# Kernel optimization log

Measured on AMD Instinct MI355X. Metric: run time of the kernel, lower is better.

The kernel has to match this reference:

```python
import jax, jax.numpy as jnp
import numpy as np

N, D, C, P = 4096, 512, 100, 64
EPS_COS = 1e-8   # torch cosine_similarity norm clamp
EPS_INV = 1e-5   # module's 1/(d + 1e-5)


def setup_inputs() -> dict:
    key = jax.random.key(0)
    k1, k2, k3, k4 = jax.random.split(key, 4)
    feats = jax.random.normal(k1, (N, D), dtype=jnp.float32)
    protos = jax.random.normal(k2, (C, P, D), dtype=jnp.float32)
    cls_ids = jax.random.randint(k3, (N,), 0, C)
    proto_labels = jax.random.randint(k4, (C, P), 0, 1000)
    return {"feats": feats, "protos": protos, "cls_ids": cls_ids,
            "proto_labels": proto_labels}


def reference(feats, protos, cls_ids, proto_labels):
    # Gather each box's class-conditional prototype set: [N, P, D]
    p = protos[cls_ids]
    pl = proto_labels[cls_ids]                       # [N, P]

    # cosine distance: 1 - f.p / (max(|f|,eps) * max(|p|,eps))
    dot = jnp.einsum('nd,npd->np', feats, p)         # [N, P]
    fnorm = jnp.maximum(jnp.linalg.norm(feats, axis=-1, keepdims=True), EPS_COS)
    pnorm = jnp.maximum(jnp.linalg.norm(p, axis=-1), EPS_COS)
    d_cos = 1.0 - dot / (fnorm * pnorm)

    diff = feats[:, None, :] - p                     # [N, P, D]
    d_l1 = jnp.mean(jnp.abs(diff), axis=-1)          # F.l1_loss (mean)
    d_l2 = jnp.mean(diff * diff, axis=-1)            # F.mse_loss (mean)

    dists = jnp.stack([d_cos, d_l1, d_l2], axis=1)   # [N, 3, P]
    probs = jax.nn.softmax(1.0 / (dists + EPS_INV), axis=-1).mean(axis=1)  # [N, P]

    idx = jnp.argmax(probs, axis=-1)                 # [N]
    labels = jnp.take_along_axis(pl, idx[:, None], axis=1)[:, 0]
    return labels, probs
```

## Files before the change

### kernel.cpp

```cpp
#include <hip/hip_runtime.h>

#define D 512
#define P 64
#define WPB 4
#define NB 2
#define MAXC 256
#define EPS_COS 1e-8f
#define EPS_INV 1e-5f

__device__ __forceinline__ float wave_sum(float v) {
#pragma unroll
    for (int m = 32; m >= 1; m >>= 1) v += __shfl_xor(v, m, 64);
    return v;
}

__global__ __launch_bounds__(256) void proto_norm_kernel(
    const float* __restrict__ protos, float* __restrict__ pp, int rows)
{
    const int lane = threadIdx.x & 63;
    const int wave = threadIdx.x >> 6;
    const int r = blockIdx.x * WPB + wave;
    if (r >= rows) return;
    const float* row = protos + (size_t)r * D;
    const float4 a = *(const float4*)(row + lane * 4);
    const float4 b = *(const float4*)(row + 256 + lane * 4);
    float s = a.x*a.x + a.y*a.y + a.z*a.z + a.w*a.w
            + b.x*b.x + b.y*b.y + b.z*b.z + b.w*b.w;
    s = wave_sum(s);
    if (lane == 0) pp[r] = s;
}

__global__ __launch_bounds__(1024) void build_groups_kernel(
    const int* __restrict__ cls_ids, int* __restrict__ slots,
    int* __restrict__ gcount, int N, int C)
{
    __shared__ int cnt[MAXC], base[MAXC], fill[MAXC];
    __shared__ int sG;
    const int tid = threadIdx.x;
    for (int c = tid; c < C; c += 1024) { cnt[c] = 0; fill[c] = 0; }
    __syncthreads();
    for (int n = tid; n < N; n += 1024) atomicAdd(&cnt[cls_ids[n]], 1);
    __syncthreads();
    if (tid == 0) {
        int gb = 0;
        for (int c = 0; c < C; ++c) { base[c] = gb; gb += (cnt[c] + NB - 1) / NB; }
        sG = gb;
        gcount[0] = gb;
    }
    __syncthreads();
    const int G = sG;
    for (int i = tid; i < G * NB; i += 1024) slots[i] = -1;
    __syncthreads();
    for (int n = tid; n < N; n += 1024) {
        const int c = cls_ids[n];
        const int p = atomicAdd(&fill[c], 1);
        slots[base[c] * NB + p] = n;
    }
}

__device__ __forceinline__ void box_epilogue(
    float r_dot, float r_l1, float ff, float s_pp, int myp,
    float& prob_o, int& bidx_o)
{
    const float fnorm = fmaxf(sqrtf(ff),   EPS_COS);
    const float pnorm = fmaxf(sqrtf(s_pp), EPS_COS);
    const float d_cos = 1.0f - r_dot / (fnorm * pnorm);
    const float d_l1  = r_l1 * (1.0f / (float)D);
    const float d_l2  = (ff - 2.0f * r_dot + s_pp) * (1.0f / (float)D);

    float s[3];
    s[0] = 1.0f / (d_cos + EPS_INV);
    s[1] = 1.0f / (d_l1  + EPS_INV);
    s[2] = 1.0f / (d_l2  + EPS_INV);

    float prob = 0.f;
#pragma unroll
    for (int i = 0; i < 3; ++i) {
        float m = s[i];
#pragma unroll
        for (int w = 32; w >= 1; w >>= 1) m = fmaxf(m, __shfl_xor(m, w, 64));
        const float e = expf(s[i] - m);
        const float denom = wave_sum(e);
        prob += e / denom;
    }
    prob *= (1.0f / 3.0f);

    float best = prob;
    int   bidx = myp;
#pragma unroll
    for (int w = 32; w >= 1; w >>= 1) {
        const float ov = __shfl_xor(best, w, 64);
        const int   oi = __shfl_xor(bidx, w, 64);
        if (ov > best || (ov == best && oi < bidx)) { best = ov; bidx = oi; }
    }
    prob_o = prob;
    bidx_o = bidx;
}

__global__ __launch_bounds__(WPB * 64) void proto_probs_kernel(
    const float* __restrict__ feats,
    const float* __restrict__ protos,
    const int*   __restrict__ cls_ids,
    const int*   __restrict__ proto_labels,
    const float* __restrict__ ppbuf,
    const int*   __restrict__ slots,
    const int*   __restrict__ gcount,
    float* __restrict__ out,
    int N)
{
    const int lane = threadIdx.x & 63;
    const int wave = threadIdx.x >> 6;

    const int nb  = gridDim.x;
    const int q   = nb >> 3, r = nb & 7;
    const int xcd = blockIdx.x & 7, bix = blockIdx.x >> 3;
    const int swz = (xcd < r ? xcd * (q + 1) : r * (q + 1) + (xcd - r) * q) + bix;

    const int g = swz * WPB + wave;
    if (g >= gcount[0]) return;

    const int b0 = slots[g * NB + 0];
    const int b1 = slots[g * NB + 1];
    const bool v1 = (b1 >= 0);
    const int n0 = b0;
    const int n1 = v1 ? b1 : b0;

    const int cls = cls_ids[n0];
    const float* fa = feats  + (size_t)n0 * D;
    const float* fb = feats  + (size_t)n1 * D;
    const float* pr = protos + (size_t)cls * (P * D);

    const float4 a0 = *(const float4*)(fa + lane * 4);
    const float4 a1 = *(const float4*)(fa + 256 + lane * 4);
    const float4 c0 = *(const float4*)(fb + lane * 4);
    const float4 c1 = *(const float4*)(fb + 256 + lane * 4);

    float ffa = a0.x*a0.x + a0.y*a0.y + a0.z*a0.z + a0.w*a0.w
              + a1.x*a1.x + a1.y*a1.y + a1.z*a1.z + a1.w*a1.w;
    float ffb = c0.x*c0.x + c0.y*c0.y + c0.z*c0.z + c0.w*c0.w
              + c1.x*c1.x + c1.y*c1.y + c1.z*c1.z + c1.w*c1.w;
    ffa = wave_sum(ffa);
    ffb = wave_sum(ffb);

    const int jsel = (lane >> 3) & 7;
    const int gown = lane & 7;
    const bool hi32 = (lane & 32) != 0;
    const bool hi16 = (lane & 16) != 0;
    const bool hi8  = (lane & 8)  != 0;

    float rdA = 0.f, rlA = 0.f, rdB = 0.f, rlB = 0.f;

    for (int gg = 0; gg < 8; ++gg) {
        float pdA[8], plA[8], pdB[8], plB[8];
#pragma unroll
        for (int j = 0; j < 8; ++j) {
            const float* row = pr + (size_t)(8 * gg + j) * D;
            const float4 q0 = *(const float4*)(row + lane * 4);
            const float4 q1 = *(const float4*)(row + 256 + lane * 4);
            float dA, lA, dB, lB, t;
            dA  = a0.x*q0.x; t = a0.x - q0.x; lA  = fabsf(t);
            dA += a0.y*q0.y; t = a0.y - q0.y; lA += fabsf(t);
            dA += a0.z*q0.z; t = a0.z - q0.z; lA += fabsf(t);
            dA += a0.w*q0.w; t = a0.w - q0.w; lA += fabsf(t);
            dA += a1.x*q1.x; t = a1.x - q1.x; lA += fabsf(t);
            dA += a1.y*q1.y; t = a1.y - q1.y; lA += fabsf(t);
            dA += a1.z*q1.z; t = a1.z - q1.z; lA += fabsf(t);
            dA += a1.w*q1.w; t = a1.w - q1.w; lA += fabsf(t);
            dB  = c0.x*q0.x; t = c0.x - q0.x; lB  = fabsf(t);
            dB += c0.y*q0.y; t = c0.y - q0.y; lB += fabsf(t);
            dB += c0.z*q0.z; t = c0.z - q0.z; lB += fabsf(t);
            dB += c0.w*q0.w; t = c0.w - q0.w; lB += fabsf(t);
            dB += c1.x*q1.x; t = c1.x - q1.x; lB += fabsf(t);
            dB += c1.y*q1.y; t = c1.y - q1.y; lB += fabsf(t);
            dB += c1.z*q1.z; t = c1.z - q1.z; lB += fabsf(t);
            dB += c1.w*q1.w; t = c1.w - q1.w; lB += fabsf(t);
            pdA[j] = dA; plA[j] = lA; pdB[j] = dB; plB[j] = lB;
        }
#pragma unroll
        for (int k = 0; k < 4; ++k) {
            const float sdA = hi32 ? pdA[k] : pdA[k + 4];
            const float slA = hi32 ? plA[k] : plA[k + 4];
            const float sdB = hi32 ? pdB[k] : pdB[k + 4];
            const float slB = hi32 ? plB[k] : plB[k + 4];
            const float rd0 = __shfl_xor(sdA, 32, 64);
            const float rl0 = __shfl_xor(slA, 32, 64);
            const float rd1 = __shfl_xor(sdB, 32, 64);
            const float rl1 = __shfl_xor(slB, 32, 64);
            pdA[k] = (hi32 ? pdA[k + 4] : pdA[k]) + rd0;
            plA[k] = (hi32 ? plA[k + 4] : plA[k]) + rl0;
            pdB[k] = (hi32 ? pdB[k + 4] : pdB[k]) + rd1;
            plB[k] = (hi32 ? plB[k + 4] : plB[k]) + rl1;
        }
#pragma unroll
        for (int k = 0; k < 2; ++k) {
            const float sdA = hi16 ? pdA[k] : pdA[k + 2];
            const float slA = hi16 ? plA[k] : plA[k + 2];
            const float sdB = hi16 ? pdB[k] : pdB[k + 2];
            const float slB = hi16 ? plB[k] : plB[k + 2];
            const float rd0 = __shfl_xor(sdA, 16, 64);
            const float rl0 = __shfl_xor(slA, 16, 64);
            const float rd1 = __shfl_xor(sdB, 16, 64);
            const float rl1 = __shfl_xor(slB, 16, 64);
            pdA[k] = (hi16 ? pdA[k + 2] : pdA[k]) + rd0;
            plA[k] = (hi16 ? plA[k + 2] : plA[k]) + rl0;
            pdB[k] = (hi16 ? pdB[k + 2] : pdB[k]) + rd1;
            plB[k] = (hi16 ? plB[k + 2] : plB[k]) + rl1;
        }
        {
            const float sdA = hi8 ? pdA[0] : pdA[1];
            const float slA = hi8 ? plA[0] : plA[1];
            const float sdB = hi8 ? pdB[0] : pdB[1];
            const float slB = hi8 ? plB[0] : plB[1];
            const float rd0 = __shfl_xor(sdA, 8, 64);
            const float rl0 = __shfl_xor(slA, 8, 64);
            const float rd1 = __shfl_xor(sdB, 8, 64);
            const float rl1 = __shfl_xor(slB, 8, 64);
            pdA[0] = (hi8 ? pdA[1] : pdA[0]) + rd0;
            plA[0] = (hi8 ? plA[1] : plA[0]) + rl0;
            pdB[0] = (hi8 ? pdB[1] : pdB[0]) + rd1;
            plB[0] = (hi8 ? plB[1] : plB[0]) + rl1;
        }
#pragma unroll
        for (int m = 4; m >= 1; m >>= 1) {
            pdA[0] += __shfl_xor(pdA[0], m, 64);
            plA[0] += __shfl_xor(plA[0], m, 64);
            pdB[0] += __shfl_xor(pdB[0], m, 64);
            plB[0] += __shfl_xor(plB[0], m, 64);
        }
        if (gown == gg) { rdA = pdA[0]; rlA = plA[0]; rdB = pdB[0]; rlB = plB[0]; }
    }

    const int myp = 8 * gown + jsel;
    const float s_pp = ppbuf[cls * P + myp];

    float probA; int bidxA;
    box_epilogue(rdA, rlA, ffa, s_pp, myp, probA, bidxA);
    out[(size_t)N + (size_t)n0 * P + myp] = probA;
    if (lane == 0) out[n0] = (float)proto_labels[cls * P + bidxA];

    if (v1) {
        float probB; int bidxB;
        box_epilogue(rdB, rlB, ffb, s_pp, myp, probB, bidxB);
        out[(size_t)N + (size_t)n1 * P + myp] = probB;
        if (lane == 0) out[n1] = (float)proto_labels[cls * P + bidxB];
    }
}

extern "C" void kernel_launch(void* const* d_in, const int* in_sizes, int n_in,
                              void* d_out, int out_size, void* d_ws, size_t ws_size,
                              hipStream_t stream) {
    const float* feats        = (const float*)d_in[0];
    const float* protos       = (const float*)d_in[1];
    const int*   cls_ids      = (const int*)d_in[2];
    const int*   proto_labels = (const int*)d_in[3];
    float* out = (float*)d_out;

    const int N    = in_sizes[2];
    const int rows = in_sizes[1] / D;
    const int C    = rows / P;

    float* pp     = (float*)d_ws;
    int*   gcount = (int*)((char*)d_ws + (size_t)rows * sizeof(float));
    int*   slots  = gcount + 1;

    const int Gmax    = (N + C * (NB - 1)) / NB;
    const int mblocks = (Gmax + WPB - 1) / WPB;

    proto_norm_kernel<<<(rows + WPB - 1) / WPB, WPB * 64, 0, stream>>>(
        protos, pp, rows);
    build_groups_kernel<<<1, 1024, 0, stream>>>(cls_ids, slots, gcount, N, C);
    proto_probs_kernel<<<mblocks, WPB * 64, 0, stream>>>(
        feats, protos, cls_ids, proto_labels, pp, slots, gcount, out, N);
}
```

Measured before the change: 119.2 us.

## Split each box-pair's D dimension across two waves and merge prep kernels

The prototype-norm and grouping kernels are fused into one launch, with the grouping block using a parallel prefix scan instead of a serial loop. The main kernel now assigns two waves to each box pair, each handling half of D, and combines their partial dot, L1 and norm sums through shared memory after a block barrier. This doubles the number of waves working on the same total work, reducing per-wave latency and register pressure. It also removes one kernel launch, at the cost of a __syncthreads and shared-memory exchange.

Measured after the change: 130.8 us. +9.7%, slower.

```diff
diff --git a/kernel.cpp b/kernel.cpp
--- a/kernel.cpp
+++ b/kernel.cpp
@@ -4,6 +4,7 @@
 #define P 64
 #define WPB 4
 #define NB 2
+#define PPB 2
 #define MAXC 256
 #define EPS_COS 1e-8f
 #define EPS_INV 1e-5f
@@ -14,47 +15,54 @@
     return v;
 }
 
-__global__ __launch_bounds__(256) void proto_norm_kernel(
-    const float* __restrict__ protos, float* __restrict__ pp, int rows)
+__global__ __launch_bounds__(256) void prep_kernel(
+    const float* __restrict__ protos, float* __restrict__ pp, int rows,
+    const int* __restrict__ cls_ids, int* __restrict__ slots,
+    int* __restrict__ gcount, int N, int C, int normBlocks)
 {
-    const int lane = threadIdx.x & 63;
-    const int wave = threadIdx.x >> 6;
-    const int r = blockIdx.x * WPB + wave;
-    if (r >= rows) return;
-    const float* row = protos + (size_t)r * D;
-    const float4 a = *(const float4*)(row + lane * 4);
-    const float4 b = *(const float4*)(row + 256 + lane * 4);
-    float s = a.x*a.x + a.y*a.y + a.z*a.z + a.w*a.w
-            + b.x*b.x + b.y*b.y + b.z*b.z + b.w*b.w;
-    s = wave_sum(s);
-    if (lane == 0) pp[r] = s;
-}
-
-__global__ __launch_bounds__(1024) void build_groups_kernel(
-    const int* __restrict__ cls_ids, int* __restrict__ slots,
-    int* __restrict__ gcount, int N, int C)
-{
-    __shared__ int cnt[MAXC], base[MAXC], fill[MAXC];
-    __shared__ int sG;
+    if ((int)blockIdx.x < normBlocks) {
+        const int lane = threadIdx.x & 63;
+        const int wave = threadIdx.x >> 6;
+        const int r = blockIdx.x * WPB + wave;
+        if (r >= rows) return;
+        const float* row = protos + (size_t)r * D;
+        const float4 a = *(const float4*)(row + lane * 4);
+        const float4 b = *(const float4*)(row + 256 + lane * 4);
+        float s = a.x*a.x + a.y*a.y + a.z*a.z + a.w*a.w
+                + b.x*b.x + b.y*b.y + b.z*b.z + b.w*b.w;
+        s = wave_sum(s);
+        if (lane == 0) pp[r] = s;
+        return;
+    }
+
+    __shared__ int cnt[MAXC], bas[MAXC], fil[MAXC];
+    __shared__ int sv[256];
     const int tid = threadIdx.x;
-    for (int c = tid; c < C; c += 1024) { cnt[c] = 0; fill[c] = 0; }
-    __syncthreads();
-    for (int n = tid; n < N; n += 1024) atomicAdd(&cnt[cls_ids[n]], 1);
-    __syncthreads();
-    if (tid == 0) {
-        int gb = 0;
-        for (int c = 0; c < C; ++c) { base[c] = gb; gb += (cnt[c] + NB - 1) / NB; }
-        sG = gb;
-        gcount[0] = gb;
-    }
-    __syncthreads();
-    const int G = sG;
-    for (int i = tid; i < G * NB; i += 1024) slots[i] = -1;
-    __syncthreads();
-    for (int n = tid; n < N; n += 1024) {
+    for (int c = tid; c < MAXC; c += 256) { cnt[c] = 0; fil[c] = 0; }
+    __syncthreads();
+    for (int n = tid; n < N; n += 256) atomicAdd(&cnt[cls_ids[n]], 1);
+    __syncthreads();
+    int v = 0;
+    if (tid < C) v = (cnt[tid] + NB - 1) / NB;
+    sv[tid] = v;
+    __syncthreads();
+#pragma unroll
+    for (int off = 1; off < 256; off <<= 1) {
+        const int t = (tid >= off) ? sv[tid - off] : 0;
+        __syncthreads();
+        sv[tid] += t;
+        __syncthreads();
+    }
+    const int G = sv[255];
+    if (tid < C) bas[tid] = sv[tid] - v;
+    if (tid == 0) gcount[0] = G;
+    __syncthreads();
+    for (int i = tid; i < G * NB; i += 256) slots[i] = -1;
+    __syncthreads();
+    for (int n = tid; n < N; n += 256) {
         const int c = cls_ids[n];
-        const int p = atomicAdd(&fill[c], 1);
-        slots[base[c] * NB + p] = n;
+        const int p = atomicAdd(&fil[c], 1);
+        slots[bas[c] * NB + p] = n;
     }
 }
 
@@ -97,7 +105,7 @@
     bidx_o = bidx;
 }
 
-__global__ __launch_bounds__(WPB * 64) void proto_probs_kernel(
+__global__ __launch_bounds__(PPB * 2 * 64) void proto_probs_kernel(
     const float* __restrict__ feats,
     const float* __restrict__ protos,
     const int*   __restrict__ cls_ids,
@@ -108,39 +116,24 @@
     float* __restrict__ out,
     int N)
 {
-    const int lane = threadIdx.x & 63;
-    const int wave = threadIdx.x >> 6;
-
-    const int nb  = gridDim.x;
-    const int q   = nb >> 3, r = nb & 7;
+    const int lane   = threadIdx.x & 63;
+    const int wave   = threadIdx.x >> 6;
+    const int pairId = wave >> 1;
+    const int sub    = wave & 1;
+
+    const int nbk = gridDim.x;
+    const int q   = nbk >> 3, r = nbk & 7;
     const int xcd = blockIdx.x & 7, bix = blockIdx.x >> 3;
     const int swz = (xcd < r ? xcd * (q + 1) : r * (q + 1) + (xcd - r) * q) + bix;
 
-    const int g = swz * WPB + wave;
-    if (g >= gcount[0]) return;
-
-    const int b0 = slots[g * NB + 0];
-    const int b1 = slots[g * NB + 1];
-    const bool v1 = (b1 >= 0);
-    const int n0 = b0;
-    const int n1 = v1 ? b1 : b0;
-
-    const int cls = cls_ids[n0];
-    const float* fa = feats  + (size_t)n0 * D;
-    const float* fb = feats  + (size_t)n1 * D;
-    const float* pr = protos + (size_t)cls * (P * D);
-
-    const float4 a0 = *(const float4*)(fa + lane * 4);
-    const float4 a1 = *(const float4*)(fa + 256 + lane * 4);
-    const float4 c0 = *(const float4*)(fb + lane * 4);
-    const float4 c1 = *(const float4*)(fb + 256 + lane * 4);
-
-    float ffa = a0.x*a0.x + a0.y*a0.y + a0.z*a0.z + a0.w*a0.w
-              + a1.x*a1.x + a1.y*a1.y + a1.z*a1.z + a1.w*a1.w;
-    float ffb = c0.x*c0.x + c0.y*c0.y + c0.z*c0.z + c0.w*c0.w
-              + c1.x*c1.x + c1.y*c1.y + c1.z*c1.z + c1.w*c1.w;
-    ffa = wave_sum(ffa);
-    ffb = wave_sum(ffb);
+    const int g = swz * PPB + pairId;
+    const int G = gcount[0];
+    int b0 = -1, b1 = -1;
+    if (g < G) { b0 = slots[NB * g]; b1 = slots[NB * g + 1]; }
+    const bool act = (b0 >= 0);
+    const bool v1  = (b1 >= 0);
+    const int n0 = act ? b0 : 0;
+    const int n1 = v1 ? b1 : n0;
 
     const int jsel = (lane >> 3) & 7;
     const int gown = lane & 7;
@@ -148,101 +141,119 @@
     const bool hi16 = (lane & 16) != 0;
     const bool hi8  = (lane & 8)  != 0;
 
-    float rdA = 0.f, rlA = 0.f, rdB = 0.f, rlB = 0.f;
-
-    for (int gg = 0; gg < 8; ++gg) {
-        float pdA[8], plA[8], pdB[8], plB[8];
-#pragma unroll
-        for (int j = 0; j < 8; ++j) {
-            const float* row = pr + (size_t)(8 * gg + j) * D;
-            const float4 q0 = *(const float4*)(row + lane * 4);
-            const float4 q1 = *(const float4*)(row + 256 + lane * 4);
-            float dA, lA, dB, lB, t;
-            dA  = a0.x*q0.x; t = a0.x - q0.x; lA  = fabsf(t);
-            dA += a0.y*q0.y; t = a0.y - q0.y; lA += fabsf(t);
-            dA += a0.z*q0.z; t = a0.z - q0.z; lA += fabsf(t);
-            dA += a0.w*q0.w; t = a0.w - q0.w; lA += fabsf(t);
-            dA += a1.x*q1.x; t = a1.x - q1.x; lA += fabsf(t);
-            dA += a1.y*q1.y; t = a1.y - q1.y; lA += fabsf(t);
-            dA += a1.z*q1.z; t = a1.z - q1.z; lA += fabsf(t);
-            dA += a1.w*q1.w; t = a1.w - q1.w; lA += fabsf(t);
-            dB  = c0.x*q0.x; t = c0.x - q0.x; lB  = fabsf(t);
-            dB += c0.y*q0.y; t = c0.y - q0.y; lB += fabsf(t);
-            dB += c0.z*q0.z; t = c0.z - q0.z; lB += fabsf(t);
-            dB += c0.w*q0.w; t = c0.w - q0.w; lB += fabsf(t);
-            dB += c1.x*q1.x; t = c1.x - q1.x; lB += fabsf(t);
-            dB += c1.y*q1.y; t = c1.y - q1.y; lB += fabsf(t);
-            dB += c1.z*q1.z; t = c1.z - q1.z; lB += fabsf(t);
-            dB += c1.w*q1.w; t = c1.w - q1.w; lB += fabsf(t);
-            pdA[j] = dA; plA[j] = lA; pdB[j] = dB; plB[j] = lB;
+    float rdA = 0.f, rlA = 0.f, rdB = 0.f, rlB = 0.f, ffa = 0.f, ffb = 0.f;
+    int cls = 0;
+
+    __shared__ float4 xch[PPB][2][64];
+    __shared__ float  xff[PPB][2][2];
+
+    if (act) {
+        cls = cls_ids[n0];
+        const float* fa = feats  + (size_t)n0 * D + sub * (D / 2);
+        const float* fb = feats  + (size_t)n1 * D + sub * (D / 2);
+        const float* pr = protos + (size_t)cls * (P * D) + sub * (D / 2);
+
+        const float4 a0 = *(const float4*)(fa + lane * 4);
+        const float4 c0 = *(const float4*)(fb + lane * 4);
+        ffa = wave_sum(a0.x*a0.x + a0.y*a0.y + a0.z*a0.z + a0.w*a0.w);
+        ffb = wave_sum(c0.x*c0.x + c0.y*c0.y + c0.z*c0.z + c0.w*c0.w);
+
+        for (int gg = 0; gg < 8; ++gg) {
+            float pdA[8], plA[8], pdB[8], plB[8];
+#pragma unroll
+            for (int j = 0; j < 8; ++j) {
+                const float* row = pr + (size_t)(8 * gg + j) * D;
+                const float4 q0 = *(const float4*)(row + lane * 4);
+                float dA, lA, dB, lB, t;
+                dA  = a0.x*q0.x; t = a0.x - q0.x; lA  = fabsf(t);
+                dA += a0.y*q0.y; t = a0.y - q0.y; lA += fabsf(t);
+                dA += a0.z*q0.z; t = a0.z - q0.z; lA += fabsf(t);
+                dA += a0.w*q0.w; t = a0.w - q0.w; lA += fabsf(t);
+                dB  = c0.x*q0.x; t = c0.x - q0.x; lB  = fabsf(t);
+                dB += c0.y*q0.y; t = c0.y - q0.y; lB += fabsf(t);
+                dB += c0.z*q0.z; t = c0.z - q0.z; lB += fabsf(t);
+                dB += c0.w*q0.w; t = c0.w - q0.w; lB += fabsf(t);
+                pdA[j] = dA; plA[j] = lA; pdB[j] = dB; plB[j] = lB;
+            }
+#pragma unroll
+            for (int k = 0; k < 4; ++k) {
+                const float sdA = hi32 ? pdA[k] : pdA[k + 4];
+                const float slA = hi32 ? plA[k] : plA[k + 4];
+                const float sdB = hi32 ? pdB[k] : pdB[k + 4];
+                const float slB = hi32 ? plB[k] : plB[k + 4];
+                const float rd0 = __shfl_xor(sdA, 32, 64);
+                const float rl0 = __shfl_xor(slA, 32, 64);
+                const float rd1 = __shfl_xor(sdB, 32, 64);
+                const float rl1 = __shfl_xor(slB, 32, 64);
+                pdA[k] = (hi32 ? pdA[k + 4] : pdA[k]) + rd0;
+                plA[k] = (hi32 ? plA[k + 4] : plA[k]) + rl0;
+                pdB[k] = (hi32 ? pdB[k + 4] : pdB[k]) + rd1;
+                plB[k] = (hi32 ? plB[k + 4] : plB[k]) + rl1;
+            }
+#pragma unroll
+            for (int k = 0; k < 2; ++k) {
+                const float sdA = hi16 ? pdA[k] : pdA[k + 2];
+                const float slA = hi16 ? plA[k] : plA[k + 2];
+                const float sdB = hi16 ? pdB[k] : pdB[k + 2];
+                const float slB = hi16 ? plB[k] : plB[k + 2];
+                const float rd0 = __shfl_xor(sdA, 16, 64);
+                const float rl0 = __shfl_xor(slA, 16, 64);
+                const float rd1 = __shfl_xor(sdB, 16, 64);
+                const float rl1 = __shfl_xor(slB, 16, 64);
+                pdA[k] = (hi16 ? pdA[k + 2] : pdA[k]) + rd0;
+                plA[k] = (hi16 ? plA[k + 2] : plA[k]) + rl0;
+                pdB[k] = (hi16 ? pdB[k + 2] : pdB[k]) + rd1;
+                plB[k] = (hi16 ? plB[k + 2] : plB[k]) + rl1;
+            }
+            {
+                const float sdA = hi8 ? pdA[0] : pdA[1];
+                const float slA = hi8 ? plA[0] : plA[1];
+                const float sdB = hi8 ? pdB[0] : pdB[1];
+                const float slB = hi8 ? plB[0] : plB[1];
+                const float rd0 = __shfl_xor(sdA, 8, 64);
+                const float rl0 = __shfl_xor(slA, 8, 64);
+                const float rd1 = __shfl_xor(sdB, 8, 64);
+                const float rl1 = __shfl_xor(slB, 8, 64);
+                pdA[0] = (hi8 ? pdA[1] : pdA[0]) + rd0;
+                plA[0] = (hi8 ? plA[1] : plA[0]) + rl0;
+                pdB[0] = (hi8 ? pdB[1] : pdB[0]) + rd1;
+                plB[0] = (hi8 ? plB[1] : plB[0]) + rl1;
+            }
+#pragma unroll
+            for (int m = 4; m >= 1; m >>= 1) {
+                pdA[0] += __shfl_xor(pdA[0], m, 64);
+                plA[0] += __shfl_xor(plA[0], m, 64);
+                pdB[0] += __shfl_xor(pdB[0], m, 64);
+                plB[0] += __shfl_xor(plB[0], m, 64);
+            }
+            if (gown == gg) { rdA = pdA[0]; rlA = plA[0]; rdB = pdB[0]; rlB = plB[0]; }
         }
-#pragma unroll
-        for (int k = 0; k < 4; ++k) {
-            const float sdA = hi32 ? pdA[k] : pdA[k + 4];
-            const float slA = hi32 ? plA[k] : plA[k + 4];
-            const float sdB = hi32 ? pdB[k] : pdB[k + 4];
-            const float slB = hi32 ? plB[k] : plB[k + 4];
-            const float rd0 = __shfl_xor(sdA, 32, 64);
-            const float rl0 = __shfl_xor(slA, 32, 64);
-            const float rd1 = __shfl_xor(sdB, 32, 64);
-            const float rl1 = __shfl_xor(slB, 32, 64);
-            pdA[k] = (hi32 ? pdA[k + 4] : pdA[k]) + rd0;
-            plA[k] = (hi32 ? plA[k + 4] : plA[k]) + rl0;
-            pdB[k] = (hi32 ? pdB[k + 4] : pdB[k]) + rd1;
-            plB[k] = (hi32 ? plB[k + 4] : plB[k]) + rl1;
-        }
-#pragma unroll
-        for (int k = 0; k < 2; ++k) {
-            const float sdA = hi16 ? pdA[k] : pdA[k + 2];
-            const float slA = hi16 ? plA[k] : plA[k + 2];
-            const float sdB = hi16 ? pdB[k] : pdB[k + 2];
-            const float slB = hi16 ? plB[k] : plB[k + 2];
-            const float rd0 = __shfl_xor(sdA, 16, 64);
-            const float rl0 = __shfl_xor(slA, 16, 64);
-            const float rd1 = __shfl_xor(sdB, 16, 64);
-            const float rl1 = __shfl_xor(slB, 16, 64);
-            pdA[k] = (hi16 ? pdA[k + 2] : pdA[k]) + rd0;
-            plA[k] = (hi16 ? plA[k + 2] : plA[k]) + rl0;
-            pdB[k] = (hi16 ? pdB[k + 2] : pdB[k]) + rd1;
-            plB[k] = (hi16 ? plB[k + 2] : plB[k]) + rl1;
-        }
-        {
-            const float sdA = hi8 ? pdA[0] : pdA[1];
-            const float slA = hi8 ? plA[0] : plA[1];
-            const float sdB = hi8 ? pdB[0] : pdB[1];
-            const float slB = hi8 ? plB[0] : plB[1];
-            const float rd0 = __shfl_xor(sdA, 8, 64);
-            const float rl0 = __shfl_xor(slA, 8, 64);
-            const float rd1 = __shfl_xor(sdB, 8, 64);
-            const float rl1 = __shfl_xor(slB, 8, 64);
-            pdA[0] = (hi8 ? pdA[1] : pdA[0]) + rd0;
-            plA[0] = (hi8 ? plA[1] : plA[0]) + rl0;
-            pdB[0] = (hi8 ? pdB[1] : pdB[0]) + rd1;
-            plB[0] = (hi8 ? plB[1] : plB[0]) + rl1;
-        }
-#pragma unroll
-        for (int m = 4; m >= 1; m >>= 1) {
-            pdA[0] += __shfl_xor(pdA[0], m, 64);
-            plA[0] += __shfl_xor(plA[0], m, 64);
-            pdB[0] += __shfl_xor(pdB[0], m, 64);
-            plB[0] += __shfl_xor(plB[0], m, 64);
-        }
-        if (gown == gg) { rdA = pdA[0]; rlA = plA[0]; rdB = pdB[0]; rlB = plB[0]; }
-    }
+
+        xch[pairId][sub][lane] = make_float4(rdA, rlA, rdB, rlB);
+        if (lane == 0) { xff[pairId][sub][0] = ffa; xff[pairId][sub][1] = ffb; }
+    }
+
+    __syncthreads();
+    if (!act) return;
+
+    const float4 o = xch[pairId][sub ^ 1][lane];
+    rdA += o.x; rlA += o.y; rdB += o.z; rlB += o.w;
+    const float ffA = xff[pairId][0][0] + xff[pairId][1][0];
+    const float ffB = xff[pairId][0][1] + xff[pairId][1][1];
 
     const int myp = 8 * gown + jsel;
     const float s_pp = ppbuf[cls * P + myp];
 
-    float probA; int bidxA;
-    box_epilogue(rdA, rlA, ffa, s_pp, myp, probA, bidxA);
-    out[(size_t)N + (size_t)n0 * P + myp] = probA;
-    if (lane == 0) out[n0] = (float)proto_labels[cls * P + bidxA];
-
-    if (v1) {
-        float probB; int bidxB;
-        box_epilogue(rdB, rlB, ffb, s_pp, myp, probB, bidxB);
-        out[(size_t)N + (size_t)n1 * P + myp] = probB;
-        if (lane == 0) out[n1] = (float)proto_labels[cls * P + bidxB];
+    if (sub == 0) {
+        float prob; int bidx;
+        box_epilogue(rdA, rlA, ffA, s_pp, myp, prob, bidx);
+        out[(size_t)N + (size_t)n0 * P + myp] = prob;
+        if (lane == 0) out[n0] = (float)proto_labels[cls * P + bidx];
+    } else if (v1) {
+        float prob; int bidx;
+        box_epilogue(rdB, rlB, ffB, s_pp, myp, prob, bidx);
+        out[(size_t)N + (size_t)n1 * P + myp] = prob;
+        if (lane == 0) out[n1] = (float)proto_labels[cls * P + bidx];
     }
 }
 
@@ -263,12 +274,12 @@
     int*   gcount = (int*)((char*)d_ws + (size_t)rows * sizeof(float));
     int*   slots  = gcount + 1;
 
-    const int Gmax    = (N + C * (NB - 1)) / NB;
-    const int mblocks = (Gmax + WPB - 1) / WPB;
-
-    proto_norm_kernel<<<(rows + WPB - 1) / WPB, WPB * 64, 0, stream>>>(
-        protos, pp, rows);
-    build_groups_kernel<<<1, 1024, 0, stream>>>(cls_ids, slots, gcount, N, C);
-    proto_probs_kernel<<<mblocks, WPB * 64, 0, stream>>>(
+    const int normBlocks = (rows + WPB - 1) / WPB;
+    const int Gmax       = (N + C * (NB - 1)) / NB;
+    const int pairBlocks = (Gmax + PPB - 1) / PPB;
+
+    prep_kernel<<<normBlocks + 1, 256, 0, stream>>>(
+        protos, pp, rows, cls_ids, slots, gcount, N, C, normBlocks);
+    proto_probs_kernel<<<pairBlocks, PPB * 2 * 64, 0, stream>>>(
         feats, protos, cls_ids, proto_labels, pp, slots, gcount, out, N);
 }
```
